# Optimization experiments

Hardware: AMD Instinct MI355X
Metric: run time of the kernel (lower is better)

Reference implementation:

```python
import jax, jax.numpy as jnp
import numpy as np
from jax import lax

DDELTA = 0.001
COEFF = 1.0 / (4.0 * DDELTA)  # 250.0
PAD = 1


def _conv(x, w):
    # x: [B,Cin,H,W], w: [Cout,Cin,kh,kw] -> [B,Cout,H,W] (same padding)
    return lax.conv_general_dilated(x, w, (1, 1), [(PAD, PAD), (PAD, PAD)],
                                    dimension_numbers=("NCHW", "OIHW", "NCHW"))


def _cconv(xr, xi, wr, wi, br, bi):
    # complex conv: (xr + i xi) * (wr + i wi) + (br + i bi)
    yr = _conv(xr, wr) - _conv(xi, wi) + br[None, :, None, None]
    yi = _conv(xr, wi) + _conv(xi, wr) + bi[None, :, None, None]
    return yr, yi


def _sigma(x):
    # smooth ReLU: relu outside |x|<=ddelta, quadratic blend inside
    return jnp.where(jnp.abs(x) > DDELTA,
                     jax.nn.relu(x),
                     x * x * COEFF + 0.5 * x + 0.25 * DDELTA)


def setup_inputs() -> dict:
    key = jax.random.key(0)
    ks = jax.random.split(key, 16)
    B, F, H, W = 2, 48, 320, 320
    d = {
        "x_real": jax.random.normal(ks[0], (B, 1, H, W), jnp.float32),
        "x_imag": jax.random.normal(ks[1], (B, 1, H, W), jnp.float32),
        "w0_real": jax.random.normal(ks[2], (F, 1, 3, 3), jnp.float32) * 0.2,
        "w0_imag": jax.random.normal(ks[3], (F, 1, 3, 3), jnp.float32) * 0.2,
        "b0_real": jax.random.normal(ks[4], (F,), jnp.float32) * 0.05,
        "b0_imag": jax.random.normal(ks[5], (F,), jnp.float32) * 0.05,
        "w1_real": jax.random.normal(ks[6], (F, F, 3, 3), jnp.float32) * 0.05,
        "w1_imag": jax.random.normal(ks[7], (F, F, 3, 3), jnp.float32) * 0.05,
        "b1_real": jax.random.normal(ks[8], (F,), jnp.float32) * 0.05,
        "b1_imag": jax.random.normal(ks[9], (F,), jnp.float32) * 0.05,
        "w2_real": jax.random.normal(ks[10], (F, F, 3, 3), jnp.float32) * 0.05,
        "w2_imag": jax.random.normal(ks[11], (F, F, 3, 3), jnp.float32) * 0.05,
        "b2_real": jax.random.normal(ks[12], (F,), jnp.float32) * 0.05,
        "b2_imag": jax.random.normal(ks[13], (F,), jnp.float32) * 0.05,
    }
    return d


def reference(x_real, x_imag,
              w0_real, w0_imag, b0_real, b0_imag,
              w1_real, w1_imag, b1_real, b1_imag,
              w2_real, w2_imag, b2_real, b2_imag):
    # layer 0: conv only (no activation before first conv)
    r, i = _cconv(x_real, x_imag, w0_real, w0_imag, b0_real, b0_imag)
    cache = [(r, i)]
    for (wr, wi, br, bi) in ((w1_real, w1_imag, b1_real, b1_imag),
                             (w2_real, w2_imag, b2_real, b2_imag)):
        ar, ai = _sigma(r), _sigma(i)  # activation applied separately to real/imag
        r, i = _cconv(ar, ai, wr, wi, br, bi)
        cache.append((r, i))
    # cache list of complex tensors -> stacked real repr [n_convs, B, F, H, W, 2]
    return jnp.stack([jnp.stack([cr, ci], axis=-1) for cr, ci in cache], axis=0)
```

## Files before the change

kernel.cpp:

```cpp
#include <hip/hip_runtime.h>

typedef __attribute__((ext_vector_type(8))) short short8;
typedef __attribute__((ext_vector_type(4))) float f32x4;

#define IMG_H 320
#define IMG_W 320
#define NBATCH 2
#define NFEAT 48
#define PLANE (IMG_H * IMG_W)
#define KDIM 864
#define NDIM 96

#define TH 8
#define TW 32
#define FI 4
#define BLK 512
#define HALO_H (TH + 2)
#define HALO_W (TW + 2)
#define HALO_PIX (HALO_H * HALO_W)
#define CPAD 104
#define NCHUNK 12
#define STAGE_TOT (HALO_PIX * NCHUNK)
#define ETS 33

__device__ __forceinline__ float sigma_f(float x) {
    float ax = __builtin_fabsf(x);
    float quad = x * x * 250.0f + 0.5f * x + 0.00025f;
    float rel = fmaxf(x, 0.0f);
    return ax > 0.001f ? rel : quad;
}

__device__ __forceinline__ unsigned short f2bf(float f) {
    union { float f; unsigned u; } v; v.f = f;
    unsigned r = (v.u + 0x7FFFu + ((v.u >> 16) & 1u)) >> 16;
    return (unsigned short)r;
}

__device__ __forceinline__ void wprep_piece(
    int idx,
    const float* __restrict__ wr1, const float* __restrict__ wi1,
    const float* __restrict__ wr2, const float* __restrict__ wi2,
    unsigned short* __restrict__ wt1, unsigned short* __restrict__ wt2) {
    if (idx >= 2 * NDIM * KDIM) return;
    int which = idx >= NDIM * KDIM;
    int id = which ? idx - NDIM * KDIM : idx;
    const float* wr = which ? wr2 : wr1;
    const float* wi = which ? wi2 : wi1;
    unsigned short* wt = which ? wt2 : wt1;
    int n = id / KDIM;
    int k = id - n * KDIM;
    int tap = k / 96;
    int cp = k - tap * 96;
    int f = (n < 48) ? n : n - 48;
    int c = (cp < 48) ? cp : cp - 48;
    int widx = (f * 48 + c) * 9 + tap;
    float v;
    if (n < 48) v = (cp < 48) ?  wr[widx] : -wi[widx];
    else        v = (cp < 48) ?  wi[widx] :  wr[widx];
    wt[id] = f2bf(v);
}

template<int OUT_NHWC>
__global__ __launch_bounds__(256) void layer0_kernel(
    const float* __restrict__ xr, const float* __restrict__ xi,
    const float* __restrict__ wr, const float* __restrict__ wi,
    const float* __restrict__ br, const float* __restrict__ bi,
    const float* __restrict__ w1r, const float* __restrict__ w1i,
    const float* __restrict__ w2r, const float* __restrict__ w2i,
    unsigned short* __restrict__ wt1, unsigned short* __restrict__ wt2,
    float* __restrict__ out, unsigned short* __restrict__ nhwc) {
    int idx = blockIdx.x * 256 + threadIdx.x;
    wprep_piece(idx, w1r, w1i, w2r, w2i, wt1, wt2);

    int b = idx / PLANE;
    int p = idx - b * PLANE;
    int h = p / IMG_W;
    int w = p - h * IMG_W;
    const float* xrp = xr + (size_t)b * PLANE;
    const float* xip = xi + (size_t)b * PLANE;

    float ar[9], ai[9];
#pragma unroll
    for (int dy = 0; dy < 3; ++dy) {
#pragma unroll
        for (int dx = 0; dx < 3; ++dx) {
            int hh = h + dy - 1, ww = w + dx - 1;
            bool ok = ((unsigned)hh < (unsigned)IMG_H) && ((unsigned)ww < (unsigned)IMG_W);
            ar[dy * 3 + dx] = ok ? xrp[hh * IMG_W + ww] : 0.0f;
            ai[dy * 3 + dx] = ok ? xip[hh * IMG_W + ww] : 0.0f;
        }
    }

    short8 nh[12];
#pragma unroll
    for (int f = 0; f < NFEAT; ++f) {
        float yr = br[f], yi = bi[f];
#pragma unroll
        for (int t = 0; t < 9; ++t) {
            float wrv = wr[f * 9 + t], wiv = wi[f * 9 + t];
            yr += ar[t] * wrv - ai[t] * wiv;
            yi += ar[t] * wiv + ai[t] * wrv;
        }
        float2 o; o.x = yr; o.y = yi;
        *reinterpret_cast<float2*>(out + ((size_t)(b * NFEAT + f) * PLANE + p) * 2) = o;
        if (OUT_NHWC) {
            nh[f >> 3][f & 7] = (short)f2bf(sigma_f(yr));
            nh[6 + (f >> 3)][f & 7] = (short)f2bf(sigma_f(yi));
        }
    }
    if (OUT_NHWC) {
        unsigned short* dst = nhwc + (size_t)(b * PLANE + p) * 96;
#pragma unroll
        for (int c = 0; c < 12; ++c)
            *reinterpret_cast<short8*>(dst + c * 8) = nh[c];
    }
}

template<int IN_MODE, int OUT_NHWC>
__global__ __launch_bounds__(BLK, 4) void cconv_kernel(
    const float* __restrict__ inF, const unsigned short* __restrict__ inH,
    const unsigned short* __restrict__ wt,
    const float* __restrict__ br, const float* __restrict__ bi,
    float* __restrict__ outF, unsigned short* __restrict__ outH) {
    __shared__ __align__(16) unsigned short tile[HALO_PIX * CPAD];

    int bid0 = blockIdx.x;
    int bid = (bid0 & 7) * 100 + (bid0 >> 3);
    int wblk = bid % (IMG_W / TW);
    int t = bid / (IMG_W / TW);
    int hblk = t % (IMG_H / TH);
    int b = t / (IMG_H / TH);
    int h0 = hblk * TH, w0 = wblk * TW;

    int tid = threadIdx.x;

    if (IN_MODE == 1) {
        const unsigned short* inHb = inH + (size_t)b * PLANE * 96;
        short8 v[8];
        int dst[8];
#pragma unroll
        for (int s = 0; s < 8; ++s) {
            int it = tid + s * BLK;
            int pix = it / NCHUNK;
            int chunk = it - pix * NCHUNK;
            int hh = pix / HALO_W;
            int ww = pix - hh * HALO_W;
            int h = h0 + hh - 1, w = w0 + ww - 1;
            bool inimg = ((unsigned)h < (unsigned)IMG_H) && ((unsigned)w < (unsigned)IMG_W);
            bool live = it < STAGE_TOT;
            dst[s] = live ? (pix * CPAD + chunk * 8) : -1;
            if (live && inimg)
                v[s] = *reinterpret_cast<const short8*>(
                    inHb + ((size_t)(h * IMG_W + w) * 96 + chunk * 8));
            else
                v[s] = (short8){0, 0, 0, 0, 0, 0, 0, 0};
        }
#pragma unroll
        for (int s = 0; s < 8; ++s)
            if (dst[s] >= 0) *reinterpret_cast<short8*>(&tile[dst[s]]) = v[s];
    } else {
        const float* inFb = inF + (size_t)b * NFEAT * PLANE * 2;
        for (int it = tid; it < STAGE_TOT; it += BLK) {
            int pix = it / NCHUNK;
            int chunk = it - pix * NCHUNK;
            int hh = pix / HALO_W;
            int ww = pix - hh * HALO_W;
            int h = h0 + hh - 1, w = w0 + ww - 1;
            bool ok = ((unsigned)h < (unsigned)IMG_H) && ((unsigned)w < (unsigned)IMG_W);
            int c0 = chunk * 8;
            short8 v;
#pragma unroll
            for (int j = 0; j < 8; ++j) {
                int cp = c0 + j;
                int c = (cp < 48) ? cp : cp - 48;
                int ri = (cp < 48) ? 0 : 1;
                float x = ok ? inFb[((size_t)c * PLANE + h * IMG_W + w) * 2 + ri] : 0.0f;
                v[j] = (short)f2bf(sigma_f(x));
            }
            *reinterpret_cast<short8*>(&tile[pix * CPAD + chunk * 8]) = v;
        }
    }
    __syncthreads();

    int wave = tid >> 6, lane = tid & 63;
    int wm = wave >> 1, wn = wave & 1;
    int lrow = lane & 15, lk = lane >> 4;

    int basepix[FI];
#pragma unroll
    for (int fi = 0; fi < FI; ++fi) {
        int m = wm * (FI * 16) + fi * 16 + lrow;
        basepix[fi] = (m >> 5) * HALO_W + (m & 31);
    }

    const unsigned short* wrow[3];
#pragma unroll
    for (int nf = 0; nf < 3; ++nf)
        wrow[nf] = wt + (size_t)(wn * 48 + nf * 16 + lrow) * KDIM + lk * 8;

    f32x4 acc[FI][3];
#pragma unroll
    for (int fi = 0; fi < FI; ++fi)
#pragma unroll
        for (int nf = 0; nf < 3; ++nf)
            acc[fi][nf] = (f32x4){0.f, 0.f, 0.f, 0.f};

    short8 bf[2][3];
#pragma unroll
    for (int nf = 0; nf < 3; ++nf)
        bf[0][nf] = *reinterpret_cast<const short8*>(wrow[nf]);

#pragma unroll
    for (int it = 0; it < 27; ++it) {
        const int cur = it & 1;
        const int tap = it / 3, cb = it - tap * 3;
        if (it < 26) {
            const int it2 = it + 1;
            const int tap2 = it2 / 3, cb2 = it2 - tap2 * 3;
#pragma unroll
            for (int nf = 0; nf < 3; ++nf)
                bf[cur ^ 1][nf] = *reinterpret_cast<const short8*>(wrow[nf] + tap2 * 96 + cb2 * 32);
        }
        const int tapoff = (tap / 3) * HALO_W + (tap % 3);
#pragma unroll
        for (int fi = 0; fi < FI; ++fi) {
            short8 a = *reinterpret_cast<const short8*>(
                &tile[(basepix[fi] + tapoff) * CPAD + cb * 32 + lk * 8]);
#pragma unroll
            for (int nf = 0; nf < 3; ++nf)
                acc[fi][nf] = __builtin_amdgcn_mfma_f32_16x16x32_bf16(a, bf[cur][nf], acc[fi][nf], 0, 0, 0);
        }
    }

#pragma unroll
    for (int nf = 0; nf < 3; ++nf) {
        int f = nf * 16 + lrow;
        float bias = wn ? bi[f] : br[f];
#pragma unroll
        for (int fi = 0; fi < FI; ++fi)
#pragma unroll
            for (int j = 0; j < 4; ++j)
                acc[fi][nf][j] += bias;
    }

    float* tf = reinterpret_cast<float*>(tile);
    int fl = tid >> 5;
    int p0 = tid & 31;
    int ep = tid >> 1;
    int ehf = tid & 1;
    short8 nh[6];
    __syncthreads();

#pragma unroll
    for (int r = 0; r < 3; ++r) {
        int np = wn * 16 + lrow;
#pragma unroll
        for (int fi = 0; fi < FI; ++fi) {
            int m0 = wm * (FI * 16) + fi * 16 + lk * 4;
#pragma unroll
            for (int j = 0; j < 4; ++j)
                tf[(m0 + j) * ETS + np] = acc[fi][r][j];
        }
        __syncthreads();
        float* obase = outF + (((size_t)(b * NFEAT + r * 16 + fl) * IMG_H + h0) * IMG_W + w0) * 2;
#pragma unroll
        for (int g = 0; g < TH; ++g) {
            float2 o;
            o.x = tf[(g * 32 + p0) * ETS + fl];
            o.y = tf[(g * 32 + p0) * ETS + 16 + fl];
            *reinterpret_cast<float2*>(obase + ((size_t)g * IMG_W + p0) * 2) = o;
        }
        if (OUT_NHWC) {
#pragma unroll
            for (int ci = 0; ci < 2; ++ci) {
                short8 v;
#pragma unroll
                for (int u = 0; u < 8; ++u)
                    v[u] = (short)f2bf(sigma_f(tf[ep * ETS + ehf * 16 + ci * 8 + u]));
                nh[r * 2 + ci] = v;
            }
        }
        if (r < 2) __syncthreads();
    }
    if (OUT_NHWC) {
        int h = h0 + (ep >> 5), w = w0 + (ep & 31);
        unsigned short* dst = outH + (size_t)(b * PLANE + h * IMG_W + w) * 96 + ehf * 48;
#pragma unroll
        for (int c = 0; c < 6; ++c)
            *reinterpret_cast<short8*>(dst + c * 8) = nh[c];
    }
}

extern "C" void kernel_launch(void* const* d_in, const int* in_sizes, int n_in,
                              void* d_out, int out_size, void* d_ws, size_t ws_size,
                              hipStream_t stream) {
    const float* x_real  = (const float*)d_in[0];
    const float* x_imag  = (const float*)d_in[1];
    const float* w0_real = (const float*)d_in[2];
    const float* w0_imag = (const float*)d_in[3];
    const float* b0_real = (const float*)d_in[4];
    const float* b0_imag = (const float*)d_in[5];
    const float* w1_real = (const float*)d_in[6];
    const float* w1_imag = (const float*)d_in[7];
    const float* b1_real = (const float*)d_in[8];
    const float* b1_imag = (const float*)d_in[9];
    const float* w2_real = (const float*)d_in[10];
    const float* w2_imag = (const float*)d_in[11];
    const float* b2_real = (const float*)d_in[12];
    const float* b2_imag = (const float*)d_in[13];

    float* out = (float*)d_out;
    unsigned short* wt1 = (unsigned short*)d_ws;
    unsigned short* wt2 = wt1 + NDIM * KDIM;

    const size_t wt_bytes = (size_t)2 * NDIM * KDIM * 2;
    const size_t nhwc_elems = (size_t)NBATCH * PLANE * 96;
    const size_t need = wt_bytes + 2 * nhwc_elems * 2;
    const bool fast = ws_size >= need;

    unsigned short* nhwc0 = (unsigned short*)((char*)d_ws + wt_bytes);
    unsigned short* nhwc1 = nhwc0 + nhwc_elems;

    const size_t layer_sz = (size_t)NBATCH * NFEAT * PLANE * 2;

    const int l0_grid = NBATCH * PLANE / 256;
    const int conv_grid = NBATCH * (IMG_H / TH) * (IMG_W / TW);

    if (fast) {
        layer0_kernel<1><<<l0_grid, 256, 0, stream>>>(
            x_real, x_imag, w0_real, w0_imag, b0_real, b0_imag,
            w1_real, w1_imag, w2_real, w2_imag, wt1, wt2, out, nhwc0);
        cconv_kernel<1, 1><<<conv_grid, BLK, 0, stream>>>(
            nullptr, nhwc0, wt1, b1_real, b1_imag, out + layer_sz, nhwc1);
        cconv_kernel<1, 0><<<conv_grid, BLK, 0, stream>>>(
            nullptr, nhwc1, wt2, b2_real, b2_imag, out + 2 * layer_sz, nullptr);
    } else {
        layer0_kernel<0><<<l0_grid, 256, 0, stream>>>(
            x_real, x_imag, w0_real, w0_imag, b0_real, b0_imag,
            w1_real, w1_imag, w2_real, w2_imag, wt1, wt2, out, nullptr);
        cconv_kernel<0, 0><<<conv_grid, BLK, 0, stream>>>(
            out, nullptr, wt1, b1_real, b1_imag, out + layer_sz, nullptr);
        cconv_kernel<0, 0><<<conv_grid, BLK, 0, stream>>>(
            out + layer_sz, nullptr, wt2, b2_real, b2_imag, out + 2 * layer_sz, nullptr);
    }
}
```

Before: 168.4 us.

## Stage interior halo tiles via direct global-to-LDS loads with XOR-swizzled layout

For interior tiles of the bf16 NHWC input, the halo is staged with global_load_lds so data goes straight into shared memory without passing through registers. To make that work, the tile drops its padded stride (CPAD 104) for a dense 96-channel layout, and the 16-byte chunk index is XOR-swizzled with the low pixel bits to avoid LDS bank conflicts on the MFMA A-operand reads. Boundary tiles and the fp32 input path keep register staging but write the same swizzled layout. The risk is that the correctness of the wave-uniform LDS base used by global_load_lds depends on each lane's write landing at its it*8 slot.

```diff
diff --git a/kernel.cpp b/kernel.cpp
--- a/kernel.cpp
+++ b/kernel.cpp
@@ -18,7 +18,6 @@
 #define HALO_H (TH + 2)
 #define HALO_W (TW + 2)
 #define HALO_PIX (HALO_H * HALO_W)
-#define CPAD 104
 #define NCHUNK 12
 #define STAGE_TOT (HALO_PIX * NCHUNK)
 #define ETS 33
@@ -34,6 +33,13 @@
     union { float f; unsigned u; } v; v.f = f;
     unsigned r = (v.u + 0x7FFFu + ((v.u >> 16) & 1u)) >> 16;
     return (unsigned short)r;
+}
+
+__device__ __forceinline__ void gl_lds16(const unsigned short* g, unsigned short* l) {
+    __builtin_amdgcn_global_load_lds(
+        (const __attribute__((address_space(1))) unsigned int*)g,
+        (__attribute__((address_space(3))) unsigned int*)l,
+        16, 0, 0);
 }
 
 __device__ __forceinline__ void wprep_piece(
@@ -122,7 +128,7 @@
     const unsigned short* __restrict__ wt,
     const float* __restrict__ br, const float* __restrict__ bi,
     float* __restrict__ outF, unsigned short* __restrict__ outH) {
-    __shared__ __align__(16) unsigned short tile[HALO_PIX * CPAD];
+    __shared__ __align__(16) unsigned short tile[STAGE_TOT * 8];
 
     int bid0 = blockIdx.x;
     int bid = (bid0 & 7) * 100 + (bid0 >> 3);
@@ -133,51 +139,73 @@
     int h0 = hblk * TH, w0 = wblk * TW;
 
     int tid = threadIdx.x;
+    bool interior = (hblk >= 1) && (hblk <= 38) && (wblk >= 1) && (wblk <= 8);
 
     if (IN_MODE == 1) {
         const unsigned short* inHb = inH + (size_t)b * PLANE * 96;
-        short8 v[8];
-        int dst[8];
-#pragma unroll
-        for (int s = 0; s < 8; ++s) {
-            int it = tid + s * BLK;
-            int pix = it / NCHUNK;
-            int chunk = it - pix * NCHUNK;
-            int hh = pix / HALO_W;
-            int ww = pix - hh * HALO_W;
-            int h = h0 + hh - 1, w = w0 + ww - 1;
-            bool inimg = ((unsigned)h < (unsigned)IMG_H) && ((unsigned)w < (unsigned)IMG_W);
-            bool live = it < STAGE_TOT;
-            dst[s] = live ? (pix * CPAD + chunk * 8) : -1;
-            if (live && inimg)
-                v[s] = *reinterpret_cast<const short8*>(
-                    inHb + ((size_t)(h * IMG_W + w) * 96 + chunk * 8));
-            else
-                v[s] = (short8){0, 0, 0, 0, 0, 0, 0, 0};
-        }
-#pragma unroll
-        for (int s = 0; s < 8; ++s)
-            if (dst[s] >= 0) *reinterpret_cast<short8*>(&tile[dst[s]]) = v[s];
+        if (interior) {
+            int wb = tid & ~63;
+#pragma unroll
+            for (int s = 0; s < 8; ++s) {
+                int it = tid + s * BLK;
+                if (it < STAGE_TOT) {
+                    int pix = it / NCHUNK;
+                    int c = it - pix * NCHUNK;
+                    int hh = pix / HALO_W;
+                    int ww = pix - hh * HALO_W;
+                    int h = h0 + hh - 1, w = w0 + ww - 1;
+                    int sc = c ^ (pix & 3);
+                    const unsigned short* src =
+                        inHb + ((size_t)(h * IMG_W + w) * 96 + sc * 8);
+                    gl_lds16(src, &tile[(wb + s * BLK) * 8]);
+                }
+            }
+        } else {
+            short8 v[8];
+            int dst[8];
+#pragma unroll
+            for (int s = 0; s < 8; ++s) {
+                int it = tid + s * BLK;
+                int pix = it / NCHUNK;
+                int c = it - pix * NCHUNK;
+                int hh = pix / HALO_W;
+                int ww = pix - hh * HALO_W;
+                int h = h0 + hh - 1, w = w0 + ww - 1;
+                bool inimg = ((unsigned)h < (unsigned)IMG_H) && ((unsigned)w < (unsigned)IMG_W);
+                bool live = it < STAGE_TOT;
+                int sc = c ^ (pix & 3);
+                dst[s] = live ? it * 8 : -1;
+                if (live && inimg)
+                    v[s] = *reinterpret_cast<const short8*>(
+                        inHb + ((size_t)(h * IMG_W + w) * 96 + sc * 8));
+                else
+                    v[s] = (short8){0, 0, 0, 0, 0, 0, 0, 0};
+            }
+#pragma unroll
+            for (int s = 0; s < 8; ++s)
+                if (dst[s] >= 0) *reinterpret_cast<short8*>(&tile[dst[s]]) = v[s];
+        }
     } else {
         const float* inFb = inF + (size_t)b * NFEAT * PLANE * 2;
         for (int it = tid; it < STAGE_TOT; it += BLK) {
             int pix = it / NCHUNK;
-            int chunk = it - pix * NCHUNK;
+            int c = it - pix * NCHUNK;
             int hh = pix / HALO_W;
             int ww = pix - hh * HALO_W;
             int h = h0 + hh - 1, w = w0 + ww - 1;
             bool ok = ((unsigned)h < (unsigned)IMG_H) && ((unsigned)w < (unsigned)IMG_W);
-            int c0 = chunk * 8;
+            int sc = c ^ (pix & 3);
+            int c0 = sc * 8;
             short8 v;
 #pragma unroll
             for (int j = 0; j < 8; ++j) {
                 int cp = c0 + j;
-                int c = (cp < 48) ? cp : cp - 48;
+                int cc = (cp < 48) ? cp : cp - 48;
                 int ri = (cp < 48) ? 0 : 1;
-                float x = ok ? inFb[((size_t)c * PLANE + h * IMG_W + w) * 2 + ri] : 0.0f;
+                float x = ok ? inFb[((size_t)cc * PLANE + h * IMG_W + w) * 2 + ri] : 0.0f;
                 v[j] = (short)f2bf(sigma_f(x));
             }
-            *reinterpret_cast<short8*>(&tile[pix * CPAD + chunk * 8]) = v;
+            *reinterpret_cast<short8*>(&tile[it * 8]) = v;
         }
     }
     __syncthreads();
@@ -224,8 +252,9 @@
         const int tapoff = (tap / 3) * HALO_W + (tap % 3);
 #pragma unroll
         for (int fi = 0; fi < FI; ++fi) {
-            short8 a = *reinterpret_cast<const short8*>(
-                &tile[(basepix[fi] + tapoff) * CPAD + cb * 32 + lk * 8]);
+            const int p = basepix[fi] + tapoff;
+            const int kx = ((cb << 2) | lk) ^ (p & 3);
+            short8 a = *reinterpret_cast<const short8*>(&tile[p * 96 + kx * 8]);
 #pragma unroll
             for (int nf = 0; nf < 3; ++nf)
                 acc[fi][nf] = __builtin_amdgcn_mfma_f32_16x16x32_bf16(a, bf[cur][nf], acc[fi][nf], 0, 0, 0);
```

Result: no change. 170.4 us (+1.2%).

## Fuse layer-0 conv into layer-1 kernel, computing halo activations on the fly

Applied to the files above, without the earlier changes.

The layer-1 conv kernel now computes the first complex conv plus smooth-ReLU for its halo tile directly from the input images and writes bf16 activations straight into shared memory. This removes the intermediate NHWC bf16 buffer write and reread between layer 0 and layer 1. In exchange, halo pixels are recomputed redundantly per tile, and that prologue compute runs on a subset of threads before the MFMA loop. Layer 0 still runs separately to emit its fp32 output and prepare weights.

```diff
diff --git a/kernel.cpp b/kernel.cpp
--- a/kernel.cpp
+++ b/kernel.cpp
@@ -116,6 +116,175 @@
     }
 }
 
+__global__ __launch_bounds__(BLK, 4) void cconv1_fused_kernel(
+    const float* __restrict__ xr, const float* __restrict__ xi,
+    const float* __restrict__ w0r, const float* __restrict__ w0i,
+    const float* __restrict__ b0r, const float* __restrict__ b0i,
+    const unsigned short* __restrict__ wt,
+    const float* __restrict__ br, const float* __restrict__ bi,
+    float* __restrict__ outF, unsigned short* __restrict__ outH) {
+    __shared__ __align__(16) unsigned short tile[HALO_PIX * CPAD];
+
+    int bid0 = blockIdx.x;
+    int bid = (bid0 & 7) * 100 + (bid0 >> 3);
+    int wblk = bid % (IMG_W / TW);
+    int t = bid / (IMG_W / TW);
+    int hblk = t % (IMG_H / TH);
+    int b = t / (IMG_H / TH);
+    int h0 = hblk * TH, w0 = wblk * TW;
+
+    int tid = threadIdx.x;
+
+    if (tid < HALO_PIX) {
+        const float* xrp = xr + (size_t)b * PLANE;
+        const float* xip = xi + (size_t)b * PLANE;
+        int pix = tid;
+        int hh = pix / HALO_W, ww = pix - hh * HALO_W;
+        int h = h0 + hh - 1, w = w0 + ww - 1;
+        bool inimg = ((unsigned)h < (unsigned)IMG_H) && ((unsigned)w < (unsigned)IMG_W);
+        short8 av[12];
+        if (inimg) {
+            float ar[9], ai[9];
+#pragma unroll
+            for (int dy = 0; dy < 3; ++dy) {
+#pragma unroll
+                for (int dx = 0; dx < 3; ++dx) {
+                    int h2 = h + dy - 1, w2 = w + dx - 1;
+                    bool ok = ((unsigned)h2 < (unsigned)IMG_H) && ((unsigned)w2 < (unsigned)IMG_W);
+                    ar[dy * 3 + dx] = ok ? xrp[h2 * IMG_W + w2] : 0.0f;
+                    ai[dy * 3 + dx] = ok ? xip[h2 * IMG_W + w2] : 0.0f;
+                }
+            }
+#pragma unroll
+            for (int f = 0; f < NFEAT; ++f) {
+                float yr = b0r[f], yi = b0i[f];
+#pragma unroll
+                for (int tp = 0; tp < 9; ++tp) {
+                    float wrv = w0r[f * 9 + tp], wiv = w0i[f * 9 + tp];
+                    yr += ar[tp] * wrv - ai[tp] * wiv;
+                    yi += ar[tp] * wiv + ai[tp] * wrv;
+                }
+                av[f >> 3][f & 7] = (short)f2bf(sigma_f(yr));
+                av[6 + (f >> 3)][f & 7] = (short)f2bf(sigma_f(yi));
+            }
+        } else {
+#pragma unroll
+            for (int c = 0; c < 12; ++c)
+                av[c] = (short8){0, 0, 0, 0, 0, 0, 0, 0};
+        }
+#pragma unroll
+        for (int c = 0; c < 12; ++c)
+            *reinterpret_cast<short8*>(&tile[pix * CPAD + c * 8]) = av[c];
+    }
+    __syncthreads();
+
+    int wave = tid >> 6, lane = tid & 63;
+    int wm = wave >> 1, wn = wave & 1;
+    int lrow = lane & 15, lk = lane >> 4;
+
+    int basepix[FI];
+#pragma unroll
+    for (int fi = 0; fi < FI; ++fi) {
+        int m = wm * (FI * 16) + fi * 16 + lrow;
+        basepix[fi] = (m >> 5) * HALO_W + (m & 31);
+    }
+
+    const unsigned short* wrow[3];
+#pragma unroll
+    for (int nf = 0; nf < 3; ++nf)
+        wrow[nf] = wt + (size_t)(wn * 48 + nf * 16 + lrow) * KDIM + lk * 8;
+
+    f32x4 acc[FI][3];
+#pragma unroll
+    for (int fi = 0; fi < FI; ++fi)
+#pragma unroll
+        for (int nf = 0; nf < 3; ++nf)
+            acc[fi][nf] = (f32x4){0.f, 0.f, 0.f, 0.f};
+
+    short8 bf[2][3];
+#pragma unroll
+    for (int nf = 0; nf < 3; ++nf)
+        bf[0][nf] = *reinterpret_cast<const short8*>(wrow[nf]);
+
+#pragma unroll
+    for (int it = 0; it < 27; ++it) {
+        const int cur = it & 1;
+        const int tap = it / 3, cb = it - tap * 3;
+        if (it < 26) {
+            const int it2 = it + 1;
+            const int tap2 = it2 / 3, cb2 = it2 - tap2 * 3;
+#pragma unroll
+            for (int nf = 0; nf < 3; ++nf)
+                bf[cur ^ 1][nf] = *reinterpret_cast<const short8*>(wrow[nf] + tap2 * 96 + cb2 * 32);
+        }
+        const int tapoff = (tap / 3) * HALO_W + (tap % 3);
+#pragma unroll
+        for (int fi = 0; fi < FI; ++fi) {
+            short8 a = *reinterpret_cast<const short8*>(
+                &tile[(basepix[fi] + tapoff) * CPAD + cb * 32 + lk * 8]);
+#pragma unroll
+            for (int nf = 0; nf < 3; ++nf)
+                acc[fi][nf] = __builtin_amdgcn_mfma_f32_16x16x32_bf16(a, bf[cur][nf], acc[fi][nf], 0, 0, 0);
+        }
+    }
+
+#pragma unroll
+    for (int nf = 0; nf < 3; ++nf) {
+        int f = nf * 16 + lrow;
+        float bias = wn ? bi[f] : br[f];
+#pragma unroll
+        for (int fi = 0; fi < FI; ++fi)
+#pragma unroll
+            for (int j = 0; j < 4; ++j)
+                acc[fi][nf][j] += bias;
+    }
+
+    float* tf = reinterpret_cast<float*>(tile);
+    int fl = tid >> 5;
+    int p0 = tid & 31;
+    int ep = tid >> 1;
+    int ehf = tid & 1;
+    short8 nh[6];
+    __syncthreads();
+
+#pragma unroll
+    for (int r = 0; r < 3; ++r) {
+        int np = wn * 16 + lrow;
+#pragma unroll
+        for (int fi = 0; fi < FI; ++fi) {
+            int m0 = wm * (FI * 16) + fi * 16 + lk * 4;
+#pragma unroll
+            for (int j = 0; j < 4; ++j)
+                tf[(m0 + j) * ETS + np] = acc[fi][r][j];
+        }
+        __syncthreads();
+        float* obase = outF + (((size_t)(b * NFEAT + r * 16 + fl) * IMG_H + h0) * IMG_W + w0) * 2;
+#pragma unroll
+        for (int g = 0; g < TH; ++g) {
+            float2 o;
+            o.x = tf[(g * 32 + p0) * ETS + fl];
+            o.y = tf[(g * 32 + p0) * ETS + 16 + fl];
+            *reinterpret_cast<float2*>(obase + ((size_t)g * IMG_W + p0) * 2) = o;
+        }
+#pragma unroll
+        for (int ci = 0; ci < 2; ++ci) {
+            short8 v;
+#pragma unroll
+            for (int u = 0; u < 8; ++u)
+                v[u] = (short)f2bf(sigma_f(tf[ep * ETS + ehf * 16 + ci * 8 + u]));
+            nh[r * 2 + ci] = v;
+        }
+        if (r < 2) __syncthreads();
+    }
+    {
+        int h = h0 + (ep >> 5), w = w0 + (ep & 31);
+        unsigned short* dst = outH + (size_t)(b * PLANE + h * IMG_W + w) * 96 + ehf * 48;
+#pragma unroll
+        for (int c = 0; c < 6; ++c)
+            *reinterpret_cast<short8*>(dst + c * 8) = nh[c];
+    }
+}
+
 template<int IN_MODE, int OUT_NHWC>
 __global__ __launch_bounds__(BLK, 4) void cconv_kernel(
     const float* __restrict__ inF, const unsigned short* __restrict__ inH,
@@ -315,11 +484,10 @@
 
     const size_t wt_bytes = (size_t)2 * NDIM * KDIM * 2;
     const size_t nhwc_elems = (size_t)NBATCH * PLANE * 96;
-    const size_t need = wt_bytes + 2 * nhwc_elems * 2;
+    const size_t need = wt_bytes + nhwc_elems * 2;
     const bool fast = ws_size >= need;
 
-    unsigned short* nhwc0 = (unsigned short*)((char*)d_ws + wt_bytes);
-    unsigned short* nhwc1 = nhwc0 + nhwc_elems;
+    unsigned short* nhwc1 = (unsigned short*)((char*)d_ws + wt_bytes);
 
     const size_t layer_sz = (size_t)NBATCH * NFEAT * PLANE * 2;
 
@@ -327,11 +495,12 @@
     const int conv_grid = NBATCH * (IMG_H / TH) * (IMG_W / TW);
 
     if (fast) {
-        layer0_kernel<1><<<l0_grid, 256, 0, stream>>>(
+        layer0_kernel<0><<<l0_grid, 256, 0, stream>>>(
             x_real, x_imag, w0_real, w0_imag, b0_real, b0_imag,
-            w1_real, w1_imag, w2_real, w2_imag, wt1, wt2, out, nhwc0);
-        cconv_kernel<1, 1><<<conv_grid, BLK, 0, stream>>>(
-            nullptr, nhwc0, wt1, b1_real, b1_imag, out + layer_sz, nhwc1);
+            w1_real, w1_imag, w2_real, w2_imag, wt1, wt2, out, nullptr);
+        cconv1_fused_kernel<<<conv_grid, BLK, 0, stream>>>(
+            x_real, x_imag, w0_real, w0_imag, b0_real, b0_imag,
+            wt1, b1_real, b1_imag, out + layer_sz, nhwc1);
         cconv_kernel<1, 0><<<conv_grid, BLK, 0, stream>>>(
             nullptr, nhwc1, wt2, b2_real, b2_imag, out + 2 * layer_sz, nullptr);
     } else {
```

Result: slower. 185.2 us (+10.0%).
